# Kernel optimization log

Hardware: AMD Instinct MI355X
Metric: run time of the kernel (lower is better)

## Reference

```python
import jax, jax.numpy as jnp
import numpy as np
import math

B, T, D, H, E, K = 2, 2048, 1024, 16, 8, 2
F = 4 * D
HD = D // H
EPS = 1e-5


def layer_norm(x, w):
    mu = jnp.mean(x, axis=-1, keepdims=True)
    var = jnp.mean(jnp.square(x - mu), axis=-1, keepdims=True)
    return (x - mu) / jnp.sqrt(var + EPS) * w


def setup_inputs() -> dict:
    key = jax.random.key(0)
    ks = jax.random.split(key, 8)
    s = 0.02
    return {
        "x": jax.random.normal(ks[0], (B, T, D), dtype=jnp.float32),
        "ln1_w": jnp.ones((D,), dtype=jnp.float32),
        "wqkv": jax.random.normal(ks[1], (D, 3 * D), dtype=jnp.float32) * s,
        "wproj": jax.random.normal(ks[2], (D, D), dtype=jnp.float32) * s,
        "ln2_w": jnp.ones((D,), dtype=jnp.float32),
        "router_w": jax.random.normal(ks[3], (D, E), dtype=jnp.float32) * s,
        "w1": jax.random.normal(ks[4], (E, D, F), dtype=jnp.float32) * s,
        "w2": jax.random.normal(ks[5], (E, F, D), dtype=jnp.float32) * s,
    }


def reference(x, ln1_w, wqkv, wproj, ln2_w, router_w, w1, w2):
    # --- self-attention (causal, no bias, dropout=0, eval mode) ---
    h = layer_norm(x, ln1_w)
    qkv = h @ wqkv  # [B,T,3D]
    q, k, v = jnp.split(qkv, 3, axis=-1)
    q = q.reshape(B, T, H, HD).transpose(0, 2, 1, 3)  # [B,H,T,HD]
    k = k.reshape(B, T, H, HD).transpose(0, 2, 1, 3)
    v = v.reshape(B, T, H, HD).transpose(0, 2, 1, 3)
    scores = jnp.einsum("bhqd,bhkd->bhqk", q, k) / math.sqrt(HD)
    causal = jnp.tril(jnp.ones((T, T), dtype=bool))
    scores = jnp.where(causal, scores, jnp.float32(-1e9))
    attn = jax.nn.softmax(scores, axis=-1)
    o = jnp.einsum("bhqk,bhkd->bhqd", attn, v)
    o = o.transpose(0, 2, 1, 3).reshape(B, T, D) @ wproj
    x = x + o

    # --- pre-MoE norm (note: residual for MoE uses ln2 output, per source) ---
    x = layer_norm(x, ln2_w)

    # --- router (eval mode: top-k of softmax probs) ---
    logits = x @ router_w  # [B,T,E]
    probs = jax.nn.softmax(logits, axis=-1)
    _, topi = jax.lax.top_k(probs, K)  # [B,T,K]
    mask = jax.nn.one_hot(topi, E, dtype=probs.dtype).sum(axis=-2)  # [B,T,E]
    rp = probs * mask
    rp = rp / jnp.sum(rp, axis=-1, keepdims=True)  # normalize=True, top_k>1

    # --- experts: dense-equivalent of gather/MLP/scatter (zero-prob tokens contribute 0) ---
    hh = jax.nn.gelu(jnp.einsum("btd,edf->ebtf", x, w1), approximate=False)
    eo = jnp.einsum("ebtf,efd->ebtd", hh, w2)
    next_states = jnp.einsum("bte,ebtd->btd", rp, eo)
    return x + next_states
```

## Files before the change

kernel.cpp:

```cpp
#include <hip/hip_runtime.h>
#include <hip/hip_bf16.h>
#include <math.h>

#define Bv 2
#define Tv 2048
#define Dv 1024
#define Hv 16
#define Ev 8
#define Kv 2
#define Fv 4096
#define HDv 64
#define NT 4096
#define MAXTILES 72

typedef __attribute__((ext_vector_type(8))) short short8;
typedef __attribute__((ext_vector_type(4))) float f32x4;

__device__ __forceinline__ short f2bf(float f) {
  unsigned u = __builtin_bit_cast(unsigned, f);
  u += 0x7fffu + ((u >> 16) & 1u);
  return (short)(u >> 16);
}
__device__ __forceinline__ float bf2f(short s) {
  unsigned u = ((unsigned)(unsigned short)s) << 16;
  return __builtin_bit_cast(float, u);
}
__device__ __forceinline__ float wredsum(float s) {
  #pragma unroll
  for (int off = 32; off; off >>= 1) s += __shfl_down(s, off, 64);
  return s;
}
__device__ __forceinline__ void gl_lds16(const short* g, short* l) {
  __builtin_amdgcn_global_load_lds(
      (const __attribute__((address_space(1))) unsigned int*)g,
      (__attribute__((address_space(3))) unsigned int*)l, 16, 0, 0);
}

__global__ __launch_bounds__(256) void transpose_cvt(const float* __restrict__ in,
                                                     short* __restrict__ out,
                                                     int Kd, int Nd) {
  __shared__ float tile[64][65];
  const float* inb = in + (size_t)blockIdx.z * Kd * Nd;
  short* outb = out + (size_t)blockIdx.z * Kd * Nd;
  const int k0 = blockIdx.x * 64, n0 = blockIdx.y * 64;
  const int rr = threadIdx.x >> 4, cc = (threadIdx.x & 15) * 4;
  #pragma unroll
  for (int i = 0; i < 4; i++) {
    int r = rr + i * 16;
    f32x4 v = *(const f32x4*)(inb + (size_t)(k0 + r) * Nd + n0 + cc);
    tile[r][cc] = v[0]; tile[r][cc + 1] = v[1];
    tile[r][cc + 2] = v[2]; tile[r][cc + 3] = v[3];
  }
  __syncthreads();
  #pragma unroll
  for (int i = 0; i < 2; i++) {
    int e = threadIdx.x + i * 256;
    int n = e >> 3, c = (e & 7) * 8;
    short8 v;
    #pragma unroll
    for (int j = 0; j < 8; j++) v[j] = f2bf(tile[c + j][n]);
    *(short8*)(outb + (size_t)(n0 + n) * Kd + k0 + c) = v;
  }
}

__global__ __launch_bounds__(256) void vtrans_kernel(const short* __restrict__ qkv,
                                                     short* __restrict__ vT) {
  __shared__ short tile[64][72];
  const int t0 = blockIdx.x * 64;
  const int bh = blockIdx.y;
  const int b = bh >> 4, h = bh & 15;
  #pragma unroll
  for (int i = 0; i < 2; i++) {
    int e = threadIdx.x + i * 256;
    int r = e >> 3, c = (e & 7) * 8;
    short8 v = *(const short8*)(qkv + (size_t)(b * Tv + t0 + r) * 3072 + 2048 + h * 64 + c);
    *(short8*)(&tile[r][c]) = v;
  }
  __syncthreads();
  #pragma unroll
  for (int i = 0; i < 2; i++) {
    int e = threadIdx.x + i * 256;
    int d = e >> 3, c = (e & 7) * 8;
    short8 v;
    #pragma unroll
    for (int j = 0; j < 8; j++) v[j] = tile[c + j][d];
    *(short8*)(vT + ((size_t)bh * 64 + d) * Tv + t0 + c) = v;
  }
}

__global__ __launch_bounds__(256) void ln_kernel(const float* __restrict__ in,
                                                 const float* __restrict__ w,
                                                 float* __restrict__ outf,
                                                 short* __restrict__ outb) {
  int t = blockIdx.x;
  int tid = threadIdx.x;
  const float* row = in + (size_t)t * Dv;
  float v[4]; float s = 0.f;
  #pragma unroll
  for (int i = 0; i < 4; i++) { v[i] = row[tid + i * 256]; s += v[i]; }
  s = wredsum(s);
  __shared__ float red[4], red2[4];
  int wv = tid >> 6, ln = tid & 63;
  if (ln == 0) red[wv] = s;
  __syncthreads();
  float mu = (red[0] + red[1] + red[2] + red[3]) * (1.f / Dv);
  float vs = 0.f;
  #pragma unroll
  for (int i = 0; i < 4; i++) { float d = v[i] - mu; vs += d * d; }
  vs = wredsum(vs);
  if (ln == 0) red2[wv] = vs;
  __syncthreads();
  float var = (red2[0] + red2[1] + red2[2] + red2[3]) * (1.f / Dv);
  float inv = rsqrtf(var + 1e-5f);
  #pragma unroll
  for (int i = 0; i < 4; i++) {
    int d = tid + i * 256;
    float o = (v[i] - mu) * inv * w[d];
    if (outf) outf[(size_t)t * Dv + d] = o;
    if (outb) outb[(size_t)t * Dv + d] = f2bf(o);
  }
}

enum { EPI_BF16 = 0, EPI_RESID = 1, EPI_GELU = 2, EPI_F32 = 3 };

template<int EPI, bool MOE, bool INDIRECT>
__global__ __launch_bounds__(256) void gemm_lds(
    const short* __restrict__ A, const short* __restrict__ Bt,
    short* __restrict__ Cb, float* __restrict__ Cf,
    const float* __restrict__ resid,
    const int* __restrict__ perm, const int* __restrict__ tiles,
    int M, int N, int K) {
  __shared__ short As[128][32];
  __shared__ short Bs[128][32];
  int row0, row_end;
  const short* Bp = Bt;
  if (MOE) {
    int nt = tiles[0];
    if ((int)blockIdx.x >= nt) return;
    int e   = tiles[1 + blockIdx.x * 3];
    row0    = tiles[2 + blockIdx.x * 3];
    row_end = tiles[3 + blockIdx.x * 3];
    Bp = Bt + (size_t)e * K * N;
  } else {
    row0 = blockIdx.x * 128; row_end = M;
  }
  const int nbase = blockIdx.y * 128;
  const int tid = threadIdx.x;
  const int lane = tid & 63;
  const int w = tid >> 6;
  const int wm = (w >> 1) * 64, wn = (w & 1) * 64;
  const int lr = lane & 15, lk = (lane >> 4) * 8;

  const int lrow = lane >> 2, lcol = (lane & 3) * 8;
  const short* asrc[2]; short* adst[2];
  const short* bsrc[2]; short* bdst[2];
  #pragma unroll
  for (int i = 0; i < 2; i++) {
    int grow = row0 + w * 16 + i * 64 + lrow;
    if (MOE) grow = min(grow, row_end - 1);
    int arow = INDIRECT ? perm[grow] : grow;
    asrc[i] = A + (size_t)arow * K + lcol;
    adst[i] = &As[w * 16 + i * 64][0];
    bsrc[i] = Bp + (size_t)(nbase + w * 16 + i * 64 + lrow) * K + lcol;
    bdst[i] = &Bs[w * 16 + i * 64][0];
  }

  f32x4 acc[4][4];
  #pragma unroll
  for (int m = 0; m < 4; m++)
    #pragma unroll
    for (int n = 0; n < 4; n++) acc[m][n] = (f32x4)0.0f;

  for (int k0 = 0; k0 < K; k0 += 32) {
    #pragma unroll
    for (int i = 0; i < 2; i++) {
      gl_lds16(asrc[i] + k0, adst[i]);
      gl_lds16(bsrc[i] + k0, bdst[i]);
    }
    __syncthreads();
    short8 af[4], bfr[4];
    #pragma unroll
    for (int m = 0; m < 4; m++) af[m] = *(const short8*)(&As[wm + m * 16 + lr][lk]);
    #pragma unroll
    for (int n = 0; n < 4; n++) bfr[n] = *(const short8*)(&Bs[wn + n * 16 + lr][lk]);
    #pragma unroll
    for (int m = 0; m < 4; m++)
      #pragma unroll
      for (int n = 0; n < 4; n++)
        acc[m][n] = __builtin_amdgcn_mfma_f32_16x16x32_bf16(af[m], bfr[n], acc[m][n], 0, 0, 0);
    __syncthreads();
  }
  #pragma unroll
  for (int m = 0; m < 4; m++) {
    #pragma unroll
    for (int n = 0; n < 4; n++) {
      #pragma unroll
      for (int r = 0; r < 4; r++) {
        int row = row0 + wm + m * 16 + (lane >> 4) * 4 + r;
        if (MOE && row >= row_end) continue;
        int col = nbase + wn + n * 16 + lr;
        float v = acc[m][n][r];
        size_t idx = (size_t)row * N + col;
        if (EPI == EPI_BF16) {
          Cb[idx] = f2bf(v);
        } else if (EPI == EPI_RESID) {
          Cf[idx] = v + resid[idx];
        } else if (EPI == EPI_GELU) {
          float g = 0.5f * v * (1.0f + erff(v * 0.70710678118f));
          Cb[idx] = f2bf(g);
        } else {
          Cf[idx] = v;
        }
      }
    }
  }
}

#define SCL2E 0.18033688011112042f

__global__ __launch_bounds__(256) void attn_kernel(const short* __restrict__ qkv,
                                                   const short* __restrict__ vT,
                                                   short* __restrict__ o) {
  const int qbase = ((int)gridDim.x - 1 - (int)blockIdx.x) * 64;
  const int bh = blockIdx.y;
  const int b = bh >> 4, h = bh & 15;
  const int w = threadIdx.x >> 6, lane = threadIdx.x & 63;
  const int lr = lane & 15, lkg = lane >> 4, lk = lkg * 8;
  const size_t rs = 3 * Dv;

  __shared__ short Ks[64][72];
  __shared__ short Vs[64][72];
  __shared__ short Ps[4][16][72];

  short8 qf[2];
  {
    size_t qrow = (size_t)(b * Tv + qbase + w * 16 + lr) * rs + h * 64;
    qf[0] = *(const short8*)(qkv + qrow + lk);
    qf[1] = *(const short8*)(qkv + qrow + 32 + lk);
  }
  f32x4 oacc[4];
  #pragma unroll
  for (int n = 0; n < 4; n++) oacc[n] = (f32x4)0.0f;
  float mrow[4] = {-INFINITY, -INFINITY, -INFINITY, -INFINITY};
  float lrow4[4] = {0.f, 0.f, 0.f, 0.f};

  const short* kbase = qkv + (size_t)b * Tv * rs + Dv + h * 64;
  const short* vbase = vT + (size_t)bh * 64 * Tv;

  for (int kv0 = 0; kv0 < qbase + 64; kv0 += 64) {
    #pragma unroll
    for (int i = 0; i < 2; i++) {
      int e = threadIdx.x + i * 256;
      int r = e >> 3, c = (e & 7) * 8;
      short8 kval = *(const short8*)(kbase + (size_t)(kv0 + r) * rs + c);
      *(short8*)(&Ks[r][c]) = kval;
      short8 vval = *(const short8*)(vbase + (size_t)r * Tv + kv0 + c);
      *(short8*)(&Vs[r][c]) = vval;
    }
    __syncthreads();
    f32x4 s[4];
    #pragma unroll
    for (int n = 0; n < 4; n++) {
      s[n] = (f32x4)0.0f;
      short8 kf0 = *(const short8*)(&Ks[n * 16 + lr][lk]);
      short8 kf1 = *(const short8*)(&Ks[n * 16 + lr][32 + lk]);
      s[n] = __builtin_amdgcn_mfma_f32_16x16x32_bf16(qf[0], kf0, s[n], 0, 0, 0);
      s[n] = __builtin_amdgcn_mfma_f32_16x16x32_bf16(qf[1], kf1, s[n], 0, 0, 0);
    }
    if (kv0 < qbase) {
      #pragma unroll
      for (int n = 0; n < 4; n++)
        #pragma unroll
        for (int r = 0; r < 4; r++) s[n][r] *= SCL2E;
    } else {
      #pragma unroll
      for (int n = 0; n < 4; n++)
        #pragma unroll
        for (int r = 0; r < 4; r++) {
          int tq = qbase + w * 16 + lkg * 4 + r;
          int tk = kv0 + n * 16 + lr;
          s[n][r] = (tk > tq) ? -1e30f : s[n][r] * SCL2E;
        }
    }
    float scr[4];
    #pragma unroll
    for (int r = 0; r < 4; r++) {
      float m = fmaxf(fmaxf(s[0][r], s[1][r]), fmaxf(s[2][r], s[3][r]));
      #pragma unroll
      for (int off = 8; off; off >>= 1) m = fmaxf(m, __shfl_xor(m, off, 64));
      float mnew = fmaxf(mrow[r], m);
      float sc = exp2f(mrow[r] - mnew);
      float rsum = 0.f;
      #pragma unroll
      for (int n = 0; n < 4; n++) { float p = exp2f(s[n][r] - mnew); s[n][r] = p; rsum += p; }
      #pragma unroll
      for (int off = 8; off; off >>= 1) rsum += __shfl_xor(rsum, off, 64);
      lrow4[r] = lrow4[r] * sc + rsum;
      mrow[r] = mnew;
      scr[r] = sc;
    }
    #pragma unroll
    for (int n = 0; n < 4; n++)
      #pragma unroll
      for (int r = 0; r < 4; r++) Ps[w][lkg * 4 + r][n * 16 + lr] = f2bf(s[n][r]);
    #pragma unroll
    for (int n = 0; n < 4; n++)
      #pragma unroll
      for (int r = 0; r < 4; r++) oacc[n][r] *= scr[r];
    __syncthreads();
    #pragma unroll
    for (int n2 = 0; n2 < 4; n2++) {
      short8 pf0 = *(const short8*)(&Ps[w][lr][lk]);
      short8 pf1 = *(const short8*)(&Ps[w][lr][32 + lk]);
      short8 vf0 = *(const short8*)(&Vs[n2 * 16 + lr][lk]);
      short8 vf1 = *(const short8*)(&Vs[n2 * 16 + lr][32 + lk]);
      oacc[n2] = __builtin_amdgcn_mfma_f32_16x16x32_bf16(pf0, vf0, oacc[n2], 0, 0, 0);
      oacc[n2] = __builtin_amdgcn_mfma_f32_16x16x32_bf16(pf1, vf1, oacc[n2], 0, 0, 0);
    }
    __syncthreads();
  }
  float rinv[4];
  #pragma unroll
  for (int r = 0; r < 4; r++) rinv[r] = 1.0f / lrow4[r];
  #pragma unroll
  for (int n2 = 0; n2 < 4; n2++)
    #pragma unroll
    for (int r = 0; r < 4; r++) {
      int tq = qbase + w * 16 + lkg * 4 + r;
      float v = oacc[n2][r] * rinv[r];
      o[(size_t)(b * Tv + tq) * Dv + h * 64 + n2 * 16 + lr] = f2bf(v);
    }
}

__global__ __launch_bounds__(256) void router_kernel(const float* __restrict__ x2f,
                                                     const float* __restrict__ rw,
                                                     int* __restrict__ topi,
                                                     float* __restrict__ topp) {
  int w = threadIdx.x >> 6, lane = threadIdx.x & 63;
  int t = blockIdx.x * 4 + w;
  const float* row = x2f + (size_t)t * Dv;
  float acc[8];
  #pragma unroll
  for (int e = 0; e < 8; e++) acc[e] = 0.f;
  for (int i = 0; i < 16; i++) {
    int d = lane + i * 64;
    float xv = row[d];
    const float* rwp = rw + (size_t)d * 8;
    #pragma unroll
    for (int e = 0; e < 8; e++) acc[e] += xv * rwp[e];
  }
  #pragma unroll
  for (int e = 0; e < 8; e++) acc[e] = wredsum(acc[e]);
  if (lane == 0) {
    float mx = acc[0];
    #pragma unroll
    for (int e = 1; e < 8; e++) mx = fmaxf(mx, acc[e]);
    float p[8]; float se = 0.f;
    #pragma unroll
    for (int e = 0; e < 8; e++) { p[e] = expf(acc[e] - mx); se += p[e]; }
    #pragma unroll
    for (int e = 0; e < 8; e++) p[e] /= se;
    int i1 = 0; float p1 = p[0];
    #pragma unroll
    for (int e = 1; e < 8; e++) if (p[e] > p1) { p1 = p[e]; i1 = e; }
    float pm = p[i1]; p[i1] = -1.f;
    int i2 = 0; float p2 = p[0];
    #pragma unroll
    for (int e = 1; e < 8; e++) if (p[e] > p2) { p2 = p[e]; i2 = e; }
    float sum = pm + p2;
    topi[t * 2] = i1; topi[t * 2 + 1] = i2;
    topp[t * 2] = pm / sum; topp[t * 2 + 1] = p2 / sum;
  }
}

__global__ void bucket_count(const int* __restrict__ topi, int* __restrict__ offsets,
                             int* __restrict__ cursor) {
  __shared__ int cnt[8];
  if (threadIdx.x < 8) { cnt[threadIdx.x] = 0; cursor[threadIdx.x] = 0; }
  __syncthreads();
  for (int i = threadIdx.x; i < NT * 2; i += 256) atomicAdd(&cnt[topi[i]], 1);
  __syncthreads();
  if (threadIdx.x == 0) {
    int s = 0;
    for (int e = 0; e < 8; e++) { offsets[e] = s; s += cnt[e]; }
    offsets[8] = s;
  }
}
__global__ void bucket_scatter(const int* __restrict__ topi, const int* __restrict__ offsets,
                               int* __restrict__ cursor, int* __restrict__ perm,
                               int* __restrict__ row_of) {
  int i = blockIdx.x * 256 + threadIdx.x;
  if (i >= NT * 2) return;
  int e = topi[i];
  int slot = atomicAdd(&cursor[e], 1);
  int r = offsets[e] + slot;
  perm[r] = i >> 1;
  row_of[i] = r;
}
__global__ void tile_build(const int* __restrict__ offsets, int* __restrict__ tiles) {
  if (threadIdx.x == 0 && blockIdx.x == 0) {
    int nt = 0;
    for (int e = 0; e < 8; e++) {
      int r0 = offsets[e], r1 = offsets[e + 1];
      for (int m = r0; m < r1; m += 128) {
        tiles[1 + nt * 3] = e; tiles[2 + nt * 3] = m; tiles[3 + nt * 3] = r1; nt++;
      }
    }
    tiles[0] = nt;
  }
}

__global__ __launch_bounds__(256) void final_kernel(float* __restrict__ out,
                                                    const short* __restrict__ eout,
                                                    const int* __restrict__ row_of,
                                                    const float* __restrict__ topp) {
  int t = blockIdx.x; int tid = threadIdx.x;
  int r0 = row_of[t * 2], r1 = row_of[t * 2 + 1];
  float p0 = topp[t * 2], p1 = topp[t * 2 + 1];
  #pragma unroll
  for (int i = 0; i < 4; i++) {
    int d = tid + i * 256;
    out[(size_t)t * Dv + d] += p0 * bf2f(eout[(size_t)r0 * Dv + d])
                             + p1 * bf2f(eout[(size_t)r1 * Dv + d]);
  }
}

extern "C" void kernel_launch(void* const* d_in, const int* in_sizes, int n_in,
                              void* d_out, int out_size, void* d_ws, size_t ws_size,
                              hipStream_t stream) {
  const float* x        = (const float*)d_in[0];
  const float* ln1_w    = (const float*)d_in[1];
  const float* wqkv     = (const float*)d_in[2];
  const float* wproj    = (const float*)d_in[3];
  const float* ln2_w    = (const float*)d_in[4];
  const float* router_w = (const float*)d_in[5];
  const float* w1       = (const float*)d_in[6];
  const float* w2       = (const float*)d_in[7];
  float* out = (float*)d_out;
  char* ws = (char*)d_ws;

  size_t off = 0;
  short* wqkvT  = (short*)(ws + off); off += (size_t)3 * Dv * Dv * 2;
  short* wprojT = (short*)(ws + off); off += (size_t)Dv * Dv * 2;
  short* w1T    = (short*)(ws + off); off += (size_t)Ev * Dv * Fv * 2;
  short* w2T    = (short*)(ws + off); off += (size_t)Ev * Fv * Dv * 2;
  char* reg1 = ws + off; off += (size_t)NT * Dv * 2;
  short* hln1 = (short*)reg1;
  short* ob   = (short*)reg1;
  short* x2b  = (short*)reg1;
  char* reg2 = ws + off; off += (size_t)NT * 3 * Dv * 2;
  short* qkvb = (short*)reg2;
  float* xres = (float*)reg2;
  char* reg3 = ws + off; off += (size_t)NT * 2 * Fv * 2;
  short* vT = (short*)reg3;
  short* Hb = (short*)reg3;
  short* eout = (short*)(ws + off); off += (size_t)NT * 2 * Dv * 2;
  int*   topi = (int*)(ws + off);   off += NT * 2 * 4;
  float* topp = (float*)(ws + off); off += NT * 2 * 4;
  int*   offs = (int*)(ws + off);   off += 64;
  int*   cur  = (int*)(ws + off);   off += 64;
  int*   perm = (int*)(ws + off);   off += NT * 2 * 4;
  int*   rowof= (int*)(ws + off);   off += NT * 2 * 4;
  int*   tiles= (int*)(ws + off);   off += 1024;

  transpose_cvt<<<dim3(Dv / 64, 3 * Dv / 64, 1), 256, 0, stream>>>(wqkv, wqkvT, Dv, 3 * Dv);
  transpose_cvt<<<dim3(Dv / 64, Dv / 64, 1), 256, 0, stream>>>(wproj, wprojT, Dv, Dv);
  transpose_cvt<<<dim3(Dv / 64, Fv / 64, Ev), 256, 0, stream>>>(w1, w1T, Dv, Fv);
  transpose_cvt<<<dim3(Fv / 64, Dv / 64, Ev), 256, 0, stream>>>(w2, w2T, Fv, Dv);

  ln_kernel<<<NT, 256, 0, stream>>>(x, ln1_w, nullptr, hln1);
  gemm_lds<EPI_BF16, false, false><<<dim3(NT / 128, 3 * Dv / 128), 256, 0, stream>>>(
      hln1, wqkvT, qkvb, nullptr, nullptr, nullptr, nullptr, NT, 3 * Dv, Dv);
  vtrans_kernel<<<dim3(Tv / 64, Bv * Hv), 256, 0, stream>>>(qkvb, vT);
  attn_kernel<<<dim3(Tv / 64, Bv * Hv), 256, 0, stream>>>(qkvb, vT, ob);
  gemm_lds<EPI_RESID, false, false><<<dim3(NT / 128, Dv / 128), 256, 0, stream>>>(
      ob, wprojT, nullptr, xres, x, nullptr, nullptr, NT, Dv, Dv);
  ln_kernel<<<NT, 256, 0, stream>>>(xres, ln2_w, out, x2b);
  router_kernel<<<NT / 4, 256, 0, stream>>>(out, router_w, topi, topp);
  bucket_count<<<1, 256, 0, stream>>>(topi, offs, cur);
  bucket_scatter<<<NT * 2 / 256, 256, 0, stream>>>(topi, offs, cur, perm, rowof);
  tile_build<<<1, 1, 0, stream>>>(offs, tiles);
  gemm_lds<EPI_GELU, true, true><<<dim3(MAXTILES, Fv / 128), 256, 0, stream>>>(
      x2b, w1T, Hb, nullptr, nullptr, perm, tiles, 0, Fv, Dv);
  gemm_lds<EPI_BF16, true, false><<<dim3(MAXTILES, Dv / 128), 256, 0, stream>>>(
      Hb, w2T, eout, nullptr, nullptr, nullptr, tiles, 0, Dv, Fv);
  final_kernel<<<NT, 256, 0, stream>>>(out, eout, rowof, topp);
}
```

Baseline: 666.2 us.

## Double-buffer GEMM LDS tiles with BK=64 and XCD-aware block remapping

The shared GEMM kernel now uses two LDS buffers with a K-step of 64. The next tile's global-to-LDS loads are issued before computing on the current one, which halves the barriers per K element and overlaps loads with MFMA work. It also remaps workgroup IDs round-robin across the 8 XCDs so that blocks sharing B panels land on the same L2. LDS use grows fourfold, to 64 KB per block, which may cut occupancy. The remap assumes the grid size is divisible by 8.

New measurement: 752.9 us. +13.0%, slower.

```diff
diff --git a/kernel.cpp b/kernel.cpp
--- a/kernel.cpp
+++ b/kernel.cpp
@@ -124,45 +124,51 @@
 enum { EPI_BF16 = 0, EPI_RESID = 1, EPI_GELU = 2, EPI_F32 = 3 };
 
 template<int EPI, bool MOE, bool INDIRECT>
-__global__ __launch_bounds__(256) void gemm_lds(
+__global__ __launch_bounds__(256) void gemm2ph(
     const short* __restrict__ A, const short* __restrict__ Bt,
     short* __restrict__ Cb, float* __restrict__ Cf,
     const float* __restrict__ resid,
     const int* __restrict__ perm, const int* __restrict__ tiles,
     int M, int N, int K) {
-  __shared__ short As[128][32];
-  __shared__ short Bs[128][32];
+  __shared__ short As[2][128][64];
+  __shared__ short Bs[2][128][64];
+  const int nwg = gridDim.x * gridDim.y;
+  const int orig = blockIdx.y * gridDim.x + blockIdx.x;
+  const int cpx = nwg >> 3;
+  const int wgid = (orig & 7) * cpx + (orig >> 3);
+  const int mt = wgid % gridDim.x;
+  const int npan = wgid / gridDim.x;
+
   int row0, row_end;
   const short* Bp = Bt;
   if (MOE) {
-    int nt = tiles[0];
-    if ((int)blockIdx.x >= nt) return;
-    int e   = tiles[1 + blockIdx.x * 3];
-    row0    = tiles[2 + blockIdx.x * 3];
-    row_end = tiles[3 + blockIdx.x * 3];
+    int ntile = tiles[0];
+    if (mt >= ntile) return;
+    int e   = tiles[1 + mt * 3];
+    row0    = tiles[2 + mt * 3];
+    row_end = tiles[3 + mt * 3];
     Bp = Bt + (size_t)e * K * N;
   } else {
-    row0 = blockIdx.x * 128; row_end = M;
-  }
-  const int nbase = blockIdx.y * 128;
+    row0 = mt * 128; row_end = M;
+  }
+  const int nbase = npan * 128;
   const int tid = threadIdx.x;
   const int lane = tid & 63;
-  const int w = tid >> 6;
-  const int wm = (w >> 1) * 64, wn = (w & 1) * 64;
+  const int wv = tid >> 6;
+  const int wm = (wv >> 1) * 64, wn = (wv & 1) * 64;
   const int lr = lane & 15, lk = (lane >> 4) * 8;
 
-  const int lrow = lane >> 2, lcol = (lane & 3) * 8;
-  const short* asrc[2]; short* adst[2];
-  const short* bsrc[2]; short* bdst[2];
-  #pragma unroll
-  for (int i = 0; i < 2; i++) {
-    int grow = row0 + w * 16 + i * 64 + lrow;
+  const int srow = wv * 32 + (lane >> 3);
+  const int scol = (lane & 7) * 8;
+  const short* aptr[4];
+  const short* bptr[4];
+  #pragma unroll
+  for (int i = 0; i < 4; i++) {
+    int grow = row0 + srow + i * 8;
     if (MOE) grow = min(grow, row_end - 1);
     int arow = INDIRECT ? perm[grow] : grow;
-    asrc[i] = A + (size_t)arow * K + lcol;
-    adst[i] = &As[w * 16 + i * 64][0];
-    bsrc[i] = Bp + (size_t)(nbase + w * 16 + i * 64 + lrow) * K + lcol;
-    bdst[i] = &Bs[w * 16 + i * 64][0];
+    aptr[i] = A + (size_t)arow * K + scol;
+    bptr[i] = Bp + (size_t)(nbase + srow + i * 8) * K + scol;
   }
 
   f32x4 acc[4][4];
@@ -171,24 +177,38 @@
     #pragma unroll
     for (int n = 0; n < 4; n++) acc[m][n] = (f32x4)0.0f;
 
-  for (int k0 = 0; k0 < K; k0 += 32) {
-    #pragma unroll
-    for (int i = 0; i < 2; i++) {
-      gl_lds16(asrc[i] + k0, adst[i]);
-      gl_lds16(bsrc[i] + k0, bdst[i]);
+  const int KT = K >> 6;
+  #pragma unroll
+  for (int i = 0; i < 4; i++) {
+    gl_lds16(aptr[i], &As[0][wv * 32 + i * 8][0]);
+    gl_lds16(bptr[i], &Bs[0][wv * 32 + i * 8][0]);
+  }
+  __syncthreads();
+  int cur = 0;
+  for (int kt = 0; kt < KT; ++kt) {
+    if (kt + 1 < KT) {
+      const int k0 = (kt + 1) << 6;
+      #pragma unroll
+      for (int i = 0; i < 4; i++) {
+        gl_lds16(aptr[i] + k0, &As[cur ^ 1][wv * 32 + i * 8][0]);
+        gl_lds16(bptr[i] + k0, &Bs[cur ^ 1][wv * 32 + i * 8][0]);
+      }
+    }
+    #pragma unroll
+    for (int kk = 0; kk < 64; kk += 32) {
+      short8 af[4], bfr[4];
+      #pragma unroll
+      for (int m = 0; m < 4; m++) af[m] = *(const short8*)(&As[cur][wm + m * 16 + lr][kk + lk]);
+      #pragma unroll
+      for (int n = 0; n < 4; n++) bfr[n] = *(const short8*)(&Bs[cur][wn + n * 16 + lr][kk + lk]);
+      #pragma unroll
+      for (int m = 0; m < 4; m++)
+        #pragma unroll
+        for (int n = 0; n < 4; n++)
+          acc[m][n] = __builtin_amdgcn_mfma_f32_16x16x32_bf16(af[m], bfr[n], acc[m][n], 0, 0, 0);
     }
     __syncthreads();
-    short8 af[4], bfr[4];
-    #pragma unroll
-    for (int m = 0; m < 4; m++) af[m] = *(const short8*)(&As[wm + m * 16 + lr][lk]);
-    #pragma unroll
-    for (int n = 0; n < 4; n++) bfr[n] = *(const short8*)(&Bs[wn + n * 16 + lr][lk]);
-    #pragma unroll
-    for (int m = 0; m < 4; m++)
-      #pragma unroll
-      for (int n = 0; n < 4; n++)
-        acc[m][n] = __builtin_amdgcn_mfma_f32_16x16x32_bf16(af[m], bfr[n], acc[m][n], 0, 0, 0);
-    __syncthreads();
+    cur ^= 1;
   }
   #pragma unroll
   for (int m = 0; m < 4; m++) {
@@ -469,20 +489,20 @@
   transpose_cvt<<<dim3(Fv / 64, Dv / 64, Ev), 256, 0, stream>>>(w2, w2T, Fv, Dv);
 
   ln_kernel<<<NT, 256, 0, stream>>>(x, ln1_w, nullptr, hln1);
-  gemm_lds<EPI_BF16, false, false><<<dim3(NT / 128, 3 * Dv / 128), 256, 0, stream>>>(
+  gemm2ph<EPI_BF16, false, false><<<dim3(NT / 128, 3 * Dv / 128), 256, 0, stream>>>(
       hln1, wqkvT, qkvb, nullptr, nullptr, nullptr, nullptr, NT, 3 * Dv, Dv);
   vtrans_kernel<<<dim3(Tv / 64, Bv * Hv), 256, 0, stream>>>(qkvb, vT);
   attn_kernel<<<dim3(Tv / 64, Bv * Hv), 256, 0, stream>>>(qkvb, vT, ob);
-  gemm_lds<EPI_RESID, false, false><<<dim3(NT / 128, Dv / 128), 256, 0, stream>>>(
+  gemm2ph<EPI_RESID, false, false><<<dim3(NT / 128, Dv / 128), 256, 0, stream>>>(
       ob, wprojT, nullptr, xres, x, nullptr, nullptr, NT, Dv, Dv);
   ln_kernel<<<NT, 256, 0, stream>>>(xres, ln2_w, out, x2b);
   router_kernel<<<NT / 4, 256, 0, stream>>>(out, router_w, topi, topp);
   bucket_count<<<1, 256, 0, stream>>>(topi, offs, cur);
   bucket_scatter<<<NT * 2 / 256, 256, 0, stream>>>(topi, offs, cur, perm, rowof);
   tile_build<<<1, 1, 0, stream>>>(offs, tiles);
-  gemm_lds<EPI_GELU, true, true><<<dim3(MAXTILES, Fv / 128), 256, 0, stream>>>(
+  gemm2ph<EPI_GELU, true, true><<<dim3(MAXTILES, Fv / 128), 256, 0, stream>>>(
       x2b, w1T, Hb, nullptr, nullptr, perm, tiles, 0, Fv, Dv);
-  gemm_lds<EPI_BF16, true, false><<<dim3(MAXTILES, Dv / 128), 256, 0, stream>>>(
+  gemm2ph<EPI_BF16, true, false><<<dim3(MAXTILES, Dv / 128), 256, 0, stream>>>(
       Hb, w2T, eout, nullptr, nullptr, nullptr, tiles, 0, Dv, Fv);
   final_kernel<<<NT, 256, 0, stream>>>(out, eout, rowof, topp);
 }
```
